# Kernel optimization log

Measured on AMD Instinct MI355X. Metric: run time of the kernel, lower is better.

## Reference

```python
import jax, jax.numpy as jnp
import numpy as np

NUM_HEADS = 16
D_K = 64  # d_model // num_heads = 1024 // 16


def setup_inputs() -> dict:
    key = jax.random.key(0)
    ks = jax.random.split(key, 5)
    b, s, d = 2, 2048, 1024
    scale = 0.02
    return {
        "x": jax.random.normal(ks[0], (b, s, d), dtype=jnp.float32),
        "W_qkv": jax.random.normal(ks[1], (d, 3 * d), dtype=jnp.float32) * scale,
        "b_qkv": jax.random.normal(ks[2], (3 * d,), dtype=jnp.float32) * scale,
        "W_o": jax.random.normal(ks[3], (d, d), dtype=jnp.float32) * scale,
        "b_o": jax.random.normal(ks[4], (d,), dtype=jnp.float32) * scale,
    }


def reference(x, W_qkv, b_qkv, W_o, b_o):
    b, s, d = x.shape
    h, dk = NUM_HEADS, D_K
    # fused QKV projection: (b, s, 3*d_model)
    qkv = x @ W_qkv + b_qkv
    # faithful to the torch rearrange 'b s (h d)' with d = 3*d_k, then chunk:
    # each head's contiguous 3*d_k slice is split into q, k, v.
    qkv = qkv.reshape(b, s, h, 3 * dk).transpose(0, 2, 1, 3)  # (b, h, s, 3*dk)
    q, k, v = jnp.split(qkv, 3, axis=-1)  # each (b, h, s, dk)
    inv_scale = 1.0 / np.float32(np.sqrt(dk))
    scores = jnp.einsum("bhqd,bhkd->bhqk", q, k) * inv_scale  # (b, h, s, s)
    attn = jax.nn.softmax(scores, axis=-1)
    ctx = jnp.einsum("bhqk,bhkd->bhqd", attn, v)  # (b, h, s, dk)
    ctx = ctx.transpose(0, 2, 1, 3).reshape(b, s, d)  # (b, s, d_model)
    return ctx @ W_o + b_o
```

## Files before the change

### kernel.cpp

```cpp
#include <hip/hip_runtime.h>
#include <hip/hip_bf16.h>
#include <stdint.h>

#define NHEADS 16
#define DKH    64
#define BB     2
#define SS     2048
#define DM     1024
#define MROWS  (BB * SS)

typedef __attribute__((ext_vector_type(8))) short bf8_t;
typedef __attribute__((ext_vector_type(4))) float f4_t;
typedef unsigned short u16;
typedef uint32_t u32;

__device__ __forceinline__ u16 f2bf(float f) {
    union { float f; u32 u; } v; v.f = f;
    return (u16)((v.u + 0x7fffu + ((v.u >> 16) & 1u)) >> 16);
}

__device__ __forceinline__ u32 cvt_pk_bf16(float lo, float hi) {
    u32 r;
    asm("v_cvt_pk_bf16_f32 %0, %1, %2" : "=v"(r) : "v"(lo), "v"(hi));
    return r;
}

__device__ __forceinline__ float fexp2(float x) {
#if __has_builtin(__builtin_amdgcn_exp2f)
    return __builtin_amdgcn_exp2f(x);
#else
    return __expf(x * 0.69314718056f);
#endif
}

__device__ __forceinline__ void async_copy16(void* lds, const void* g) {
    __builtin_amdgcn_global_load_lds(
        (__attribute__((address_space(1))) void*)(void*)g,
        (__attribute__((address_space(3))) void*)lds, 16, 0, 0);
}

#define MFMA32(a, b, c) __builtin_amdgcn_mfma_f32_16x16x32_bf16(a, b, c, 0, 0, 0)

__global__ void k_cvt(const float* __restrict__ in, u16* __restrict__ out, int n4) {
    int stride = gridDim.x * blockDim.x;
    for (int i = blockIdx.x * blockDim.x + threadIdx.x; i < n4; i += stride) {
        float4 v = ((const float4*)in)[i];
        ushort4 o;
        o.x = f2bf(v.x); o.y = f2bf(v.y); o.z = f2bf(v.z); o.w = f2bf(v.w);
        ((ushort4*)out)[i] = o;
    }
}

__global__ void k_transpose(const float* __restrict__ W, u16* __restrict__ Wt, int K, int N) {
    __shared__ float tile[32][33];
    int n0 = blockIdx.x * 32, k0 = blockIdx.y * 32;
    int tx = threadIdx.x & 31, ty = threadIdx.x >> 5;
    #pragma unroll
    for (int r = ty; r < 32; r += 8)
        tile[r][tx] = W[(size_t)(k0 + r) * N + n0 + tx];
    __syncthreads();
    #pragma unroll
    for (int r = ty; r < 32; r += 8)
        Wt[(size_t)(n0 + r) * K + k0 + tx] = f2bf(tile[tx][r]);
}

template<int MODE>
__global__ __launch_bounds__(256) void k_gemm(
    const u16* __restrict__ A, const u16* __restrict__ Bt,
    const float* __restrict__ bias,
    u16* __restrict__ q_out, u16* __restrict__ k_out, u16* __restrict__ vt_out,
    float* __restrict__ f_out,
    int N, int K)
{
    __shared__ u16 As[128 * 32];
    __shared__ u16 Bs[128 * 32];
    const int m0 = blockIdx.y * 128, n0 = blockIdx.x * 128;
    const int tid = threadIdx.x;
    const int w = tid >> 6, l = tid & 63;
    const int lr = l >> 2, lc = (l & 3) * 8;
    const int fr = l & 15, fk = (l >> 4) * 8;
    const int wm = (w >> 1) * 64, wn = (w & 1) * 64;
    f4_t acc[4][4] = {};

    for (int kt = 0; kt < K; kt += 32) {
        #pragma unroll
        for (int cc = 0; cc < 2; ++cc) {
            const int c = w + cc * 4;
            async_copy16(As + c * 512, A  + (size_t)(m0 + c * 16 + lr) * K + kt + lc);
            async_copy16(Bs + c * 512, Bt + (size_t)(n0 + c * 16 + lr) * K + kt + lc);
        }
        __syncthreads();
        bf8_t af[4], bfr[4];
        #pragma unroll
        for (int mf = 0; mf < 4; ++mf)
            af[mf] = *(const bf8_t*)&As[(wm + mf * 16 + fr) * 32 + fk];
        #pragma unroll
        for (int nf = 0; nf < 4; ++nf)
            bfr[nf] = *(const bf8_t*)&Bs[(wn + nf * 16 + fr) * 32 + fk];
        #pragma unroll
        for (int mf = 0; mf < 4; ++mf)
            #pragma unroll
            for (int nf = 0; nf < 4; ++nf)
                acc[mf][nf] = MFMA32(af[mf], bfr[nf], acc[mf][nf]);
        __syncthreads();
    }

    #pragma unroll
    for (int mf = 0; mf < 4; ++mf)
      #pragma unroll
      for (int nf = 0; nf < 4; ++nf)
        #pragma unroll
        for (int j = 0; j < 4; ++j) {
            const int m = m0 + wm + mf * 16 + (l >> 4) * 4 + j;
            const int n = n0 + wn + nf * 16 + (l & 15);
            float v = acc[mf][nf][j] + bias[n];
            if (MODE == 0) {
                const int h = n / 192, rem = n - h * 192;
                const int which = rem >> 6, dd = rem & 63;
                const int b = m >> 11, s = m & (SS - 1);
                const u16 bv = f2bf(v);
                const size_t qk_idx = ((size_t)(b * NHEADS + h) * SS + s) * DKH + dd;
                if (which == 0)      q_out[qk_idx] = bv;
                else if (which == 1) k_out[qk_idx] = bv;
                else                 vt_out[((size_t)(b * NHEADS + h) * DKH + dd) * SS + s] = bv;
            } else {
                f_out[(size_t)m * N + n] = v;
            }
        }
}

#define SCL 0.180336880f

__global__ __launch_bounds__(256) void k_attn(
    const u16* __restrict__ Qg, const u16* __restrict__ Kg, const u16* __restrict__ Vtg,
    u16* __restrict__ ctx)
{
    __shared__ u16 Ks[64 * 64];
    __shared__ u16 Vs[64 * 64];
    const int bh = blockIdx.x;
    const int qt = blockIdx.y;
    const int tid = threadIdx.x, w = tid >> 6, l = tid & 63;
    const int fr = l & 15, fq = l >> 4;
    const int q0 = qt * 64 + w * 16;
    const u16* Qb = Qg  + (size_t)bh * SS * DKH;
    const u16* Kb = Kg  + (size_t)bh * SS * DKH;
    const u16* Vb = Vtg + (size_t)bh * DKH * SS;

    bf8_t qf[2];
    #pragma unroll
    for (int kh = 0; kh < 2; ++kh)
        qf[kh] = *(const bf8_t*)(Qb + (size_t)(q0 + fr) * DKH + kh * 32 + fq * 8);

    float mrow = -__builtin_inff(), lrow = 0.f;
    f4_t o[4] = {};

    for (int kv = 0; kv < SS; kv += 64) {
        #pragma unroll
        for (int it = 0; it < 2; ++it) {
            const int c = tid + it * 256;
            const int r = c >> 3, dslw = c & 7;
            const int sl = dslw ^ (r & 7);
            const int sr = ((r >> 2) & 3) * 16 + (r >> 4) * 4 + (r & 3);
            const int cb = it * 256 + w * 64;
            async_copy16(Ks + cb * 8, Kb + (size_t)(kv + sr) * DKH + sl * 8);
            async_copy16(Vs + cb * 8, Vb + (size_t)r * SS + kv + sl * 8);
        }
        __syncthreads();

        f4_t sa[4] = {};
        #pragma unroll
        for (int nf = 0; nf < 4; ++nf)
          #pragma unroll
          for (int kh = 0; kh < 2; ++kh) {
            const int row = nf * 16 + fr;
            const int dsl = (kh * 4 + fq) ^ (fr & 7);
            const bf8_t kb = *(const bf8_t*)&Ks[row * 64 + dsl * 8];
            sa[nf] = MFMA32(kb, qf[kh], sa[nf]);
          }

        float x = sa[0][0];
        #pragma unroll
        for (int nf = 0; nf < 4; ++nf)
          #pragma unroll
          for (int j = 0; j < 4; ++j)
            x = fmaxf(x, sa[nf][j]);
        x *= SCL;
        x = fmaxf(x, __shfl_xor(x, 16));
        x = fmaxf(x, __shfl_xor(x, 32));

        if (__any(x > mrow + 8.f)) {
            float mnew = fmaxf(mrow, x);
            float sc = fexp2(mrow - mnew);
            lrow *= sc;
            mrow = mnew;
            float sc4[4];
            #pragma unroll
            for (int j = 0; j < 4; ++j) sc4[j] = __shfl(sc, fq * 4 + j);
            #pragma unroll
            for (int df = 0; df < 4; ++df)
              #pragma unroll
              for (int j = 0; j < 4; ++j)
                o[df][j] *= sc4[j];
        }

        float ps = 0.f;
        u32 pk[8];
        #pragma unroll
        for (int nf = 0; nf < 4; ++nf) {
            float p0 = fexp2(sa[nf][0] * SCL - mrow);
            float p1 = fexp2(sa[nf][1] * SCL - mrow);
            float p2 = fexp2(sa[nf][2] * SCL - mrow);
            float p3 = fexp2(sa[nf][3] * SCL - mrow);
            ps += (p0 + p1) + (p2 + p3);
            pk[nf * 2 + 0] = cvt_pk_bf16(p0, p1);
            pk[nf * 2 + 1] = cvt_pk_bf16(p2, p3);
        }
        ps += __shfl_xor(ps, 16);
        ps += __shfl_xor(ps, 32);
        lrow += ps;

        union { bf8_t v; u32 u[4]; } pa[2];
        #pragma unroll
        for (int t = 0; t < 2; ++t) {
            pa[t].u[0] = pk[4 * t + 0]; pa[t].u[1] = pk[4 * t + 1];
            pa[t].u[2] = pk[4 * t + 2]; pa[t].u[3] = pk[4 * t + 3];
        }
        #pragma unroll
        for (int t = 0; t < 2; ++t) {
            const int dsl = (fq * 2 + t) ^ (fr & 7);
            #pragma unroll
            for (int df = 0; df < 4; ++df) {
                const bf8_t vv = *(const bf8_t*)&Vs[(df * 16 + fr) * 64 + dsl * 8];
                o[df] = MFMA32(pa[t].v, vv, o[df]);
            }
        }
        __syncthreads();
    }

    float ml[4];
    #pragma unroll
    for (int j = 0; j < 4; ++j) ml[j] = __shfl(lrow, fq * 4 + j);

    const int b = bh >> 4, h = bh & 15;
    #pragma unroll
    for (int df = 0; df < 4; ++df)
      #pragma unroll
      for (int j = 0; j < 4; ++j) {
        const int s = q0 + fq * 4 + j;
        const int dd = df * 16 + fr;
        float v = o[df][j] / ml[j];
        ctx[((size_t)(b * SS + s)) * DM + h * DKH + dd] = f2bf(v);
      }
}

extern "C" void kernel_launch(void* const* d_in, const int* in_sizes, int n_in,
                              void* d_out, int out_size, void* d_ws, size_t ws_size,
                              hipStream_t stream)
{
    const float* x     = (const float*)d_in[0];
    const float* W_qkv = (const float*)d_in[1];
    const float* b_qkv = (const float*)d_in[2];
    const float* W_o   = (const float*)d_in[3];
    const float* b_o   = (const float*)d_in[4];
    float* out = (float*)d_out;

    char* ws = (char*)d_ws;
    u16* xb   = (u16*)(ws);
    u16* Wqkt = (u16*)(ws + 8388608);
    u16* Wot  = (u16*)(ws + 8388608 + 6291456);
    u16* Qg   = (u16*)(ws + 16777216);
    u16* Kg   = Qg  + 4194304;
    u16* Vtg  = Kg  + 4194304;
    u16* ctx  = xb;

    k_cvt<<<1024, 256, 0, stream>>>(x, xb, (MROWS * DM) / 4);
    k_transpose<<<dim3(3 * DM / 32, DM / 32), 256, 0, stream>>>(W_qkv, Wqkt, DM, 3 * DM);
    k_transpose<<<dim3(DM / 32, DM / 32), 256, 0, stream>>>(W_o, Wot, DM, DM);
    k_gemm<0><<<dim3(3 * DM / 128, MROWS / 128), 256, 0, stream>>>(
        xb, Wqkt, b_qkv, Qg, Kg, Vtg, nullptr, 3 * DM, DM);
    k_attn<<<dim3(BB * NHEADS, SS / 64), 256, 0, stream>>>(Qg, Kg, Vtg, ctx);
    k_gemm<1><<<dim3(DM / 128, MROWS / 128), 256, 0, stream>>>(
        ctx, Wot, b_o, nullptr, nullptr, nullptr, out, DM, DM);
}
```

Measured before the change: 226.7 us.

## Add V transpose kernel, widen attention KV tile, shrink output GEMM tile

The QKV GEMM now writes V in row layout with coalesced stores, and a separate kernel transposes it through shared memory. Before this, V^T was produced by strided scattered stores in the GEMM epilogue. The attention kernel now processes 128 keys per iteration with a retuned swizzle, halving barriers and loop overhead, and adds an occupancy hint. The output projection GEMM switches to 64x64 tiles, giving 1024 blocks instead of 256 for better CU fill. The costs are an extra launch, an extra pass over V in memory, and more registers and LDS in attention.

```diff
diff --git a/kernel.cpp b/kernel.cpp
--- a/kernel.cpp
+++ b/kernel.cpp
@@ -64,51 +64,79 @@
         Wt[(size_t)(n0 + r) * K + k0 + tx] = f2bf(tile[tx][r]);
 }
 
-template<int MODE>
+__global__ __launch_bounds__(256) void k_vt(const u16* __restrict__ V, u16* __restrict__ Vt) {
+    __shared__ u16 t[64][72];
+    const int bh = blockIdx.y;
+    const int s0 = blockIdx.x * 64;
+    const u16* Vb = V + (size_t)bh * SS * DKH;
+    u16* Tb = Vt + (size_t)bh * DKH * SS;
+    const int tid = threadIdx.x;
+    #pragma unroll
+    for (int it = 0; it < 2; ++it) {
+        const int c = tid + it * 256;
+        const int r = c >> 3, sl = c & 7;
+        *(uint4*)&t[r][sl * 8] = *(const uint4*)(Vb + (size_t)(s0 + r) * DKH + sl * 8);
+    }
+    __syncthreads();
+    #pragma unroll
+    for (int it = 0; it < 2; ++it) {
+        const int c = tid + it * 256;
+        const int d = c >> 3, sl = c & 7;
+        uint4 o;
+        o.x = t[sl * 8 + 0][d] | ((u32)t[sl * 8 + 1][d] << 16);
+        o.y = t[sl * 8 + 2][d] | ((u32)t[sl * 8 + 3][d] << 16);
+        o.z = t[sl * 8 + 4][d] | ((u32)t[sl * 8 + 5][d] << 16);
+        o.w = t[sl * 8 + 6][d] | ((u32)t[sl * 8 + 7][d] << 16);
+        *(uint4*)(Tb + (size_t)d * SS + s0 + sl * 8) = o;
+    }
+}
+
+template<int MODE, int BMT, int BNT>
 __global__ __launch_bounds__(256) void k_gemm(
     const u16* __restrict__ A, const u16* __restrict__ Bt,
     const float* __restrict__ bias,
-    u16* __restrict__ q_out, u16* __restrict__ k_out, u16* __restrict__ vt_out,
+    u16* __restrict__ q_out, u16* __restrict__ k_out, u16* __restrict__ v_out,
     float* __restrict__ f_out,
     int N, int K)
 {
-    __shared__ u16 As[128 * 32];
-    __shared__ u16 Bs[128 * 32];
-    const int m0 = blockIdx.y * 128, n0 = blockIdx.x * 128;
+    constexpr int MF = BMT / 32, NF = BNT / 32;
+    __shared__ u16 As[BMT * 32];
+    __shared__ u16 Bs[BNT * 32];
+    const int m0 = blockIdx.y * BMT, n0 = blockIdx.x * BNT;
     const int tid = threadIdx.x;
     const int w = tid >> 6, l = tid & 63;
     const int lr = l >> 2, lc = (l & 3) * 8;
     const int fr = l & 15, fk = (l >> 4) * 8;
-    const int wm = (w >> 1) * 64, wn = (w & 1) * 64;
-    f4_t acc[4][4] = {};
+    const int wm = (w >> 1) * (BMT / 2), wn = (w & 1) * (BNT / 2);
+    f4_t acc[MF][NF] = {};
 
     for (int kt = 0; kt < K; kt += 32) {
         #pragma unroll
-        for (int cc = 0; cc < 2; ++cc) {
-            const int c = w + cc * 4;
+        for (int c = w; c < BMT / 16; c += 4)
             async_copy16(As + c * 512, A  + (size_t)(m0 + c * 16 + lr) * K + kt + lc);
+        #pragma unroll
+        for (int c = w; c < BNT / 16; c += 4)
             async_copy16(Bs + c * 512, Bt + (size_t)(n0 + c * 16 + lr) * K + kt + lc);
-        }
         __syncthreads();
-        bf8_t af[4], bfr[4];
-        #pragma unroll
-        for (int mf = 0; mf < 4; ++mf)
+        bf8_t af[MF], bfr[NF];
+        #pragma unroll
+        for (int mf = 0; mf < MF; ++mf)
             af[mf] = *(const bf8_t*)&As[(wm + mf * 16 + fr) * 32 + fk];
         #pragma unroll
-        for (int nf = 0; nf < 4; ++nf)
+        for (int nf = 0; nf < NF; ++nf)
             bfr[nf] = *(const bf8_t*)&Bs[(wn + nf * 16 + fr) * 32 + fk];
         #pragma unroll
-        for (int mf = 0; mf < 4; ++mf)
+        for (int mf = 0; mf < MF; ++mf)
             #pragma unroll
-            for (int nf = 0; nf < 4; ++nf)
+            for (int nf = 0; nf < NF; ++nf)
                 acc[mf][nf] = MFMA32(af[mf], bfr[nf], acc[mf][nf]);
         __syncthreads();
     }
 
     #pragma unroll
-    for (int mf = 0; mf < 4; ++mf)
+    for (int mf = 0; mf < MF; ++mf)
       #pragma unroll
-      for (int nf = 0; nf < 4; ++nf)
+      for (int nf = 0; nf < NF; ++nf)
         #pragma unroll
         for (int j = 0; j < 4; ++j) {
             const int m = m0 + wm + mf * 16 + (l >> 4) * 4 + j;
@@ -118,11 +146,9 @@
                 const int h = n / 192, rem = n - h * 192;
                 const int which = rem >> 6, dd = rem & 63;
                 const int b = m >> 11, s = m & (SS - 1);
-                const u16 bv = f2bf(v);
-                const size_t qk_idx = ((size_t)(b * NHEADS + h) * SS + s) * DKH + dd;
-                if (which == 0)      q_out[qk_idx] = bv;
-                else if (which == 1) k_out[qk_idx] = bv;
-                else                 vt_out[((size_t)(b * NHEADS + h) * DKH + dd) * SS + s] = bv;
+                const size_t idx = ((size_t)(b * NHEADS + h) * SS + s) * DKH + dd;
+                u16* dst = (which == 0) ? q_out : ((which == 1) ? k_out : v_out);
+                dst[idx] = f2bf(v);
             } else {
                 f_out[(size_t)m * N + n] = v;
             }
@@ -131,12 +157,12 @@
 
 #define SCL 0.180336880f
 
-__global__ __launch_bounds__(256) void k_attn(
+__global__ __launch_bounds__(256, 4) void k_attn(
     const u16* __restrict__ Qg, const u16* __restrict__ Kg, const u16* __restrict__ Vtg,
     u16* __restrict__ ctx)
 {
-    __shared__ u16 Ks[64 * 64];
-    __shared__ u16 Vs[64 * 64];
+    __shared__ u16 Ks[128 * 64];
+    __shared__ u16 Vs[64 * 128];
     const int bh = blockIdx.x;
     const int qt = blockIdx.y;
     const int tid = threadIdx.x, w = tid >> 6, l = tid & 63;
@@ -154,22 +180,24 @@
     float mrow = -__builtin_inff(), lrow = 0.f;
     f4_t o[4] = {};
 
-    for (int kv = 0; kv < SS; kv += 64) {
-        #pragma unroll
-        for (int it = 0; it < 2; ++it) {
+    for (int kv = 0; kv < SS; kv += 128) {
+        #pragma unroll
+        for (int it = 0; it < 4; ++it) {
             const int c = tid + it * 256;
-            const int r = c >> 3, dslw = c & 7;
-            const int sl = dslw ^ (r & 7);
-            const int sr = ((r >> 2) & 3) * 16 + (r >> 4) * 4 + (r & 3);
             const int cb = it * 256 + w * 64;
-            async_copy16(Ks + cb * 8, Kb + (size_t)(kv + sr) * DKH + sl * 8);
-            async_copy16(Vs + cb * 8, Vb + (size_t)r * SS + kv + sl * 8);
+            const int rk = c >> 3;
+            const int slk = (c & 7) ^ (rk & 7);
+            const int sr = ((rk >> 2) & 3) * 32 + (rk >> 4) * 4 + (rk & 3);
+            async_copy16(Ks + cb * 8, Kb + (size_t)(kv + sr) * DKH + slk * 8);
+            const int rv = c >> 4;
+            const int slv = (c & 15) ^ (rv & 7);
+            async_copy16(Vs + cb * 8, Vb + (size_t)rv * SS + kv + slv * 8);
         }
         __syncthreads();
 
-        f4_t sa[4] = {};
-        #pragma unroll
-        for (int nf = 0; nf < 4; ++nf)
+        f4_t sa[8] = {};
+        #pragma unroll
+        for (int nf = 0; nf < 8; ++nf)
           #pragma unroll
           for (int kh = 0; kh < 2; ++kh) {
             const int row = nf * 16 + fr;
@@ -180,7 +208,7 @@
 
         float x = sa[0][0];
         #pragma unroll
-        for (int nf = 0; nf < 4; ++nf)
+        for (int nf = 0; nf < 8; ++nf)
           #pragma unroll
           for (int j = 0; j < 4; ++j)
             x = fmaxf(x, sa[nf][j]);
@@ -204,9 +232,9 @@
         }
 
         float ps = 0.f;
-        u32 pk[8];
-        #pragma unroll
-        for (int nf = 0; nf < 4; ++nf) {
+        u32 pk[16];
+        #pragma unroll
+        for (int nf = 0; nf < 8; ++nf) {
             float p0 = fexp2(sa[nf][0] * SCL - mrow);
             float p1 = fexp2(sa[nf][1] * SCL - mrow);
             float p2 = fexp2(sa[nf][2] * SCL - mrow);
@@ -219,19 +247,18 @@
         ps += __shfl_xor(ps, 32);
         lrow += ps;
 
-        union { bf8_t v; u32 u[4]; } pa[2];
-        #pragma unroll
-        for (int t = 0; t < 2; ++t) {
-            pa[t].u[0] = pk[4 * t + 0]; pa[t].u[1] = pk[4 * t + 1];
-            pa[t].u[2] = pk[4 * t + 2]; pa[t].u[3] = pk[4 * t + 3];
-        }
-        #pragma unroll
-        for (int t = 0; t < 2; ++t) {
-            const int dsl = (fq * 2 + t) ^ (fr & 7);
+        #pragma unroll
+        for (int t = 0; t < 4; ++t) {
+            union { bf8_t v; u32 u[4]; } pa;
+            pa.u[0] = pk[4 * t + 0]; pa.u[1] = pk[4 * t + 1];
+            pa.u[2] = pk[4 * t + 2]; pa.u[3] = pk[4 * t + 3];
+            const int sl = fq * 4 + t;
             #pragma unroll
             for (int df = 0; df < 4; ++df) {
-                const bf8_t vv = *(const bf8_t*)&Vs[(df * 16 + fr) * 64 + dsl * 8];
-                o[df] = MFMA32(pa[t].v, vv, o[df]);
+                const int rv = df * 16 + fr;
+                const int dsl = sl ^ (rv & 7);
+                const bf8_t vv = *(const bf8_t*)&Vs[rv * 128 + dsl * 8];
+                o[df] = MFMA32(pa.v, vv, o[df]);
             }
         }
         __syncthreads();
@@ -270,15 +297,17 @@
     u16* Wot  = (u16*)(ws + 8388608 + 6291456);
     u16* Qg   = (u16*)(ws + 16777216);
     u16* Kg   = Qg  + 4194304;
-    u16* Vtg  = Kg  + 4194304;
+    u16* Vg   = Kg  + 4194304;
+    u16* Vtg  = Vg  + 4194304;
     u16* ctx  = xb;
 
     k_cvt<<<1024, 256, 0, stream>>>(x, xb, (MROWS * DM) / 4);
     k_transpose<<<dim3(3 * DM / 32, DM / 32), 256, 0, stream>>>(W_qkv, Wqkt, DM, 3 * DM);
     k_transpose<<<dim3(DM / 32, DM / 32), 256, 0, stream>>>(W_o, Wot, DM, DM);
-    k_gemm<0><<<dim3(3 * DM / 128, MROWS / 128), 256, 0, stream>>>(
-        xb, Wqkt, b_qkv, Qg, Kg, Vtg, nullptr, 3 * DM, DM);
+    k_gemm<0, 128, 128><<<dim3(3 * DM / 128, MROWS / 128), 256, 0, stream>>>(
+        xb, Wqkt, b_qkv, Qg, Kg, Vg, nullptr, 3 * DM, DM);
+    k_vt<<<dim3(SS / 64, BB * NHEADS), 256, 0, stream>>>(Vg, Vtg);
     k_attn<<<dim3(BB * NHEADS, SS / 64), 256, 0, stream>>>(Qg, Kg, Vtg, ctx);
-    k_gemm<1><<<dim3(DM / 128, MROWS / 128), 256, 0, stream>>>(
+    k_gemm<1, 64, 64><<<dim3(DM / 64, MROWS / 64), 256, 0, stream>>>(
         ctx, Wot, b_o, nullptr, nullptr, nullptr, out, DM, DM);
 }
```

Measured after the change: 198.1 us. 1.14x faster.
